# Optimization experiments

Measured on AMD Instinct MI355X. Metric: run time of the kernel, lower is better.

The kernel has to match this reference:

```python
import jax, jax.numpy as jnp
import numpy as np

TEMP = 0.7
B, V, C, H, W = 4, 2, 128, 32, 32  # V=2 views


def setup_inputs() -> dict:
    key = jax.random.key(0)
    k1, k2 = jax.random.split(key)
    feats = jax.random.normal(k1, (B, V, C, H, W), dtype=jnp.float32)
    # 'cos_dst' in the original implies L2-normalized embeddings along C
    feats = feats / jnp.linalg.norm(feats, axis=2, keepdims=True)
    labels = jax.random.randint(k2, (B, V, H, W), 0, 4, dtype=jnp.int32)
    return {"features": feats, "labels": labels}


def reference(features, labels):
    # split views on dim=1 and concat on batch (as in torch forward)
    f = jnp.concatenate([features[:, 0], features[:, 1]], axis=0)  # [2B, C, H, W]
    lab = jnp.concatenate([labels[:, 0], labels[:, 1]], axis=0)     # [2B, H, W]
    c = f.shape[1]
    # flatten pixels in (b, i, j) order -> [N, C]
    F_ = jnp.transpose(f, (0, 2, 3, 1)).reshape(-1, c)
    L_ = lab.reshape(-1)                                            # [N]
    # pairwise similarities: the triple loop's per-anchor 1x1 conv, batched
    S = jnp.einsum('nc,mc->nm', F_, F_) / TEMP                      # [N, N]
    diag = jnp.diagonal(S)                                          # self-contrast per anchor
    same = (L_[None, :] == L_[:, None]).astype(S.dtype)             # positives mask (incl. self)
    num = jnp.sum(same * S, axis=1) - diag
    den = jnp.sum(jnp.exp(S), axis=1) - jnp.exp(diag)
    cnt = jnp.sum(same, axis=1) - 1.0                               # mask.sum() - 1
    valid = (L_ != 0)                                               # x_label == 1 (label 0) skipped
    cnt_safe = jnp.where(valid, cnt, 1.0)
    loss_a = jnp.where(valid, jnp.log(den) - num / cnt_safe, 0.0)
    n_valid = jnp.sum(valid.astype(S.dtype))
    return jnp.where(n_valid > 0, jnp.sum(loss_a) / jnp.maximum(n_valid, 1.0), 0.0)
```

## Files before the change

kernel.cpp:

```cpp
#include <hip/hip_runtime.h>

#define TEMP 0.7f
#define LOG2E 1.4426950408889634f
#define LN2 0.6931471805599453f
#define NPIX 8192
#define CDIM 128
#define FSCALE 1.4356161f
#define EXPDIAG 4.1727352f

typedef __bf16 v8bf __attribute__((ext_vector_type(8)));
typedef float f32x4 __attribute__((ext_vector_type(4)));

#define OFF_ROWSUM 0
#define OFF_G      8192
#define OFF_COUNTS 8704
#define OFF_ACC    8708
#define OFF_ZERON  8712
#define OFF_SWF    8960

__global__ __launch_bounds__(256) void k0_zero(float* __restrict__ w) {
    const int i = blockIdx.x * 256 + threadIdx.x;
    if (i < OFF_ZERON) w[i] = 0.0f;
}

__global__ __launch_bounds__(256) void k1_build(
    const float* __restrict__ feats, const int* __restrict__ labels,
    v8bf* __restrict__ swf, float* __restrict__ G, int* __restrict__ counts)
{
    __shared__ float lds[128][65];
    __shared__ int lab_l[64];
    __shared__ float cs[2][4][128];

    const int t = threadIdx.x;
    const int lane = t & 63, cg = t >> 6;
    const int bp = blockIdx.x >> 4;
    const int pc = blockIdx.x & 15;
    const int b = bp & 3, v = bp >> 2;
    const int bv = b * 2 + v;
    const int p0 = pc * 64;
    const int nbase = bp * 1024 + p0;

    const float* src = feats + (size_t)bv * CDIM * 1024 + p0;
#pragma unroll
    for (int i = 0; i < 32; i++) {
        const int c = cg * 32 + i;
        lds[c][lane] = src[c * 1024 + lane];
    }
    if (t < 64) {
        const int lab = labels[bv * 1024 + p0 + t];
        lab_l[t] = lab;
#pragma unroll
        for (int k = 0; k < 4; k++) {
            unsigned long long m = __ballot(lab == k);
            if (t == 0) atomicAdd(&counts[k], (int)__popcll(m));
        }
    }
    __syncthreads();

    {
        const int cw = t & 127, h = t >> 7;
        float s0 = 0.f, s1 = 0.f, s2 = 0.f, s3 = 0.f;
#pragma unroll
        for (int i = 0; i < 32; i++) {
            const int nl = h * 32 + i;
            const int lab = lab_l[nl];
            const float f = lds[cw][nl];
            s0 += (lab == 0) ? f : 0.f;
            s1 += (lab == 1) ? f : 0.f;
            s2 += (lab == 2) ? f : 0.f;
            s3 += (lab == 3) ? f : 0.f;
        }
        cs[h][0][cw] = s0; cs[h][1][cw] = s1;
        cs[h][2][cw] = s2; cs[h][3][cw] = s3;
    }
    __syncthreads();
    if (t < 128) {
#pragma unroll
        for (int k = 0; k < 4; k++)
            atomicAdd(&G[k * CDIM + t], cs[0][k][t] + cs[1][k][t]);
    }

    #pragma unroll
    for (int i = 0; i < 4; i++) {
        const int slot = i * 256 + t;
        const int f = slot >> 6, l = slot & 63;
        const int ctl = f >> 2, kk = f & 3;
        const int q = l >> 4, r = l & 15;
        const int nl = ctl * 16 + r;
        const int c0 = kk * 32 + q * 8;
        v8bf val;
#pragma unroll
        for (int j = 0; j < 8; j++) val[j] = (__bf16)(lds[c0 + j][nl] * FSCALE);
        const int ctg = (nbase >> 4) + ctl;
        swf[(ctg * 4 + kk) * 64 + l] = val;
    }
}

__global__ __launch_bounds__(256, 4) void k3_gemm_expsum(
    const v8bf* __restrict__ swf, float* __restrict__ rowsum)
{
    const int lane = threadIdx.x & 63;
    const int wave = threadIdx.x >> 6;
    const int rowblk = blockIdx.x & 31;
    const int colchunk = blockIdx.x >> 5;
    const int rowbase = rowblk * 256 + wave * 64;
    const int rt0 = rowbase >> 4;

    v8bf a[4][4];
#pragma unroll
    for (int tt = 0; tt < 4; tt++)
#pragma unroll
        for (int kk = 0; kk < 4; kk++)
            a[tt][kk] = swf[((rt0 + tt) * 4 + kk) * 64 + lane];

    float rs[4][4];
#pragma unroll
    for (int tt = 0; tt < 4; tt++)
#pragma unroll
        for (int r = 0; r < 4; r++) rs[tt][r] = 0.f;

    const int ct0 = colchunk * 16;
    for (int ct = ct0; ct < ct0 + 16; ++ct) {
        const v8bf b0 = swf[(ct * 4 + 0) * 64 + lane];
        const v8bf b1 = swf[(ct * 4 + 1) * 64 + lane];
        const v8bf b2 = swf[(ct * 4 + 2) * 64 + lane];
        const v8bf b3 = swf[(ct * 4 + 3) * 64 + lane];
#pragma unroll
        for (int tt = 0; tt < 4; tt++) {
            f32x4 acc = {0.f, 0.f, 0.f, 0.f};
            acc = __builtin_amdgcn_mfma_f32_16x16x32_bf16(a[tt][0], b0, acc, 0, 0, 0);
            acc = __builtin_amdgcn_mfma_f32_16x16x32_bf16(a[tt][1], b1, acc, 0, 0, 0);
            acc = __builtin_amdgcn_mfma_f32_16x16x32_bf16(a[tt][2], b2, acc, 0, 0, 0);
            acc = __builtin_amdgcn_mfma_f32_16x16x32_bf16(a[tt][3], b3, acc, 0, 0, 0);
#pragma unroll
            for (int r = 0; r < 4; r++)
                rs[tt][r] += __builtin_amdgcn_exp2f(acc[r]);
        }
    }

#pragma unroll
    for (int m = 1; m < 16; m <<= 1)
#pragma unroll
        for (int tt = 0; tt < 4; tt++)
#pragma unroll
            for (int r = 0; r < 4; r++)
                rs[tt][r] += __shfl_xor(rs[tt][r], m, 64);

    if ((lane & 15) == 0) {
        const int g = lane >> 4;
#pragma unroll
        for (int tt = 0; tt < 4; tt++)
#pragma unroll
            for (int r = 0; r < 4; r++)
                atomicAdd(&rowsum[rowbase + tt * 16 + g * 4 + r], rs[tt][r]);
    }
}

__global__ __launch_bounds__(256) void k4_loss(
    const float* __restrict__ feats, const int* __restrict__ labels,
    const float* __restrict__ G, const int* __restrict__ counts,
    const float* __restrict__ rowsum, float* __restrict__ acc)
{
    __shared__ float pd[4][64];
    const int t = threadIdx.x, lane = t & 63, w = t >> 6;
    const int n0 = blockIdx.x * 64;
    const int bp = n0 >> 10, p0 = n0 & 1023;
    const int bv = ((bp & 3) << 1) + (bp >> 2);
    const int p = p0 + lane;
    const int lab = labels[(bv << 10) + p];

    const float* src = feats + (((size_t)bv * CDIM + w * 32) << 10) + p;
    const float* g0p = G + w * 32;
    float dot = 0.f;
#pragma unroll 8
    for (int c = 0; c < 32; ++c) {
        const float f = src[(size_t)c << 10];
        const float g0 = g0p[c], g1 = g0p[CDIM + c];
        const float g2 = g0p[2 * CDIM + c], g3 = g0p[3 * CDIM + c];
        const float g = (lab == 1) ? g1 : (lab == 2) ? g2 : (lab == 3) ? g3 : g0;
        dot += f * g;
    }
    pd[w][lane] = dot;
    __syncthreads();
    if (w == 0) {
        const float d = pd[0][lane] + pd[1][lane] + pd[2][lane] + pd[3][lane];
        float loss = 0.f;
        if (lab != 0) {
            const float num = (d - 1.0f) * (1.0f / TEMP);
            const float den = rowsum[n0 + lane] - EXPDIAG;
            const float cnt = (float)(counts[lab] - 1);
            loss = __builtin_amdgcn_logf(den) * LN2 - num / cnt;
        }
#pragma unroll
        for (int m = 1; m < 64; m <<= 1) loss += __shfl_xor(loss, m, 64);
        if (lane == 0) atomicAdd(acc, loss);
    }
}

__global__ void k5_final(const float* __restrict__ acc,
                         const int* __restrict__ counts,
                         float* __restrict__ out)
{
    const int nv = NPIX - counts[0];
    out[0] = (nv > 0) ? acc[0] / (float)nv : 0.0f;
}

extern "C" void kernel_launch(void* const* d_in, const int* in_sizes, int n_in,
                              void* d_out, int out_size, void* d_ws, size_t ws_size,
                              hipStream_t stream) {
    const float* feats = (const float*)d_in[0];
    const int* labels = (const int*)d_in[1];
    float* out = (float*)d_out;
    float* W = (float*)d_ws;

    float* rowsum = W + OFF_ROWSUM;
    float* G      = W + OFF_G;
    int*   counts = (int*)(W + OFF_COUNTS);
    float* acc    = W + OFF_ACC;
    v8bf*  swf    = (v8bf*)(W + OFF_SWF);

    k0_zero<<<(OFF_ZERON + 255) / 256, 256, 0, stream>>>(W);
    k1_build<<<128, 256, 0, stream>>>(feats, labels, swf, G, counts);
    k3_gemm_expsum<<<32 * 32, 256, 0, stream>>>(swf, rowsum);
    k4_loss<<<128, 256, 0, stream>>>(feats, labels, G, counts, rowsum, acc);
    k5_final<<<1, 1, 0, stream>>>(acc, counts, out);
}
```

Baseline: 47.27 us.

## Exploit Gram symmetry in exp-sum GEMM and fuse final reduction into loss kernel

The similarity-exp GEMM now covers only the upper-triangular 256x256 block pairs (528 blocks instead of 1024). Each off-diagonal block adds its exp values to both row sums and column sums via per-column shuffles and atomics, roughly halving the MFMA and exp2 work. In exchange it adds many more atomic adds and a serial loop to decode the block index. The build kernel is split into 256 blocks of 32 pixels for more parallelism. The final scalar kernel is folded into the loss kernel using a last-block-done counter, which removes one launch.

```diff
diff --git a/kernel.cpp b/kernel.cpp
--- a/kernel.cpp
+++ b/kernel.cpp
@@ -15,6 +15,7 @@
 #define OFF_G      8192
 #define OFF_COUNTS 8704
 #define OFF_ACC    8708
+#define OFF_DONE   8709
 #define OFF_ZERON  8712
 #define OFF_SWF    8960
 
@@ -27,26 +28,26 @@
     const float* __restrict__ feats, const int* __restrict__ labels,
     v8bf* __restrict__ swf, float* __restrict__ G, int* __restrict__ counts)
 {
-    __shared__ float lds[128][65];
-    __shared__ int lab_l[64];
+    __shared__ float lds[128][33];
+    __shared__ int lab_l[32];
     __shared__ float cs[2][4][128];
 
     const int t = threadIdx.x;
-    const int lane = t & 63, cg = t >> 6;
-    const int bp = blockIdx.x >> 4;
-    const int pc = blockIdx.x & 15;
+    const int bp = blockIdx.x >> 5;
+    const int pc = blockIdx.x & 31;
     const int b = bp & 3, v = bp >> 2;
     const int bv = b * 2 + v;
-    const int p0 = pc * 64;
+    const int p0 = pc * 32;
     const int nbase = bp * 1024 + p0;
 
     const float* src = feats + (size_t)bv * CDIM * 1024 + p0;
-#pragma unroll
-    for (int i = 0; i < 32; i++) {
-        const int c = cg * 32 + i;
-        lds[c][lane] = src[c * 1024 + lane];
-    }
-    if (t < 64) {
+    const int px = t & 31, c8 = t >> 5;
+#pragma unroll
+    for (int i = 0; i < 16; i++) {
+        const int c = i * 8 + c8;
+        lds[c][px] = src[c * 1024 + px];
+    }
+    if (t < 32) {
         const int lab = labels[bv * 1024 + p0 + t];
         lab_l[t] = lab;
 #pragma unroll
@@ -61,8 +62,8 @@
         const int cw = t & 127, h = t >> 7;
         float s0 = 0.f, s1 = 0.f, s2 = 0.f, s3 = 0.f;
 #pragma unroll
-        for (int i = 0; i < 32; i++) {
-            const int nl = h * 32 + i;
+        for (int i = 0; i < 16; i++) {
+            const int nl = h * 16 + i;
             const int lab = lab_l[nl];
             const float f = lds[cw][nl];
             s0 += (lab == 0) ? f : 0.f;
@@ -80,9 +81,9 @@
             atomicAdd(&G[k * CDIM + t], cs[0][k][t] + cs[1][k][t]);
     }
 
-    #pragma unroll
-    for (int i = 0; i < 4; i++) {
-        const int slot = i * 256 + t;
+#pragma unroll
+    for (int i2 = 0; i2 < 2; i2++) {
+        const int slot = i2 * 256 + t;
         const int f = slot >> 6, l = slot & 63;
         const int ctl = f >> 2, kk = f & 3;
         const int q = l >> 4, r = l & 15;
@@ -96,15 +97,19 @@
     }
 }
 
-__global__ __launch_bounds__(256, 4) void k3_gemm_expsum(
+__global__ __launch_bounds__(256, 2) void k3_gemm_expsum(
     const v8bf* __restrict__ swf, float* __restrict__ rowsum)
 {
     const int lane = threadIdx.x & 63;
     const int wave = threadIdx.x >> 6;
-    const int rowblk = blockIdx.x & 31;
-    const int colchunk = blockIdx.x >> 5;
-    const int rowbase = rowblk * 256 + wave * 64;
+    int rem = blockIdx.x, bi = 0;
+    while (rem >= 32 - bi) { rem -= 32 - bi; bi++; }
+    const int bj = bi + rem;
+    const bool offdiag = (bj != bi);
+    const int rowbase = bi * 256 + wave * 64;
+    const int colbase = bj * 256;
     const int rt0 = rowbase >> 4;
+    const int ct0 = colbase >> 4;
 
     v8bf a[4][4];
 #pragma unroll
@@ -119,12 +124,14 @@
 #pragma unroll
         for (int r = 0; r < 4; r++) rs[tt][r] = 0.f;
 
-    const int ct0 = colchunk * 16;
-    for (int ct = ct0; ct < ct0 + 16; ++ct) {
+#pragma unroll
+    for (int cl = 0; cl < 16; ++cl) {
+        const int ct = ct0 + cl;
         const v8bf b0 = swf[(ct * 4 + 0) * 64 + lane];
         const v8bf b1 = swf[(ct * 4 + 1) * 64 + lane];
         const v8bf b2 = swf[(ct * 4 + 2) * 64 + lane];
         const v8bf b3 = swf[(ct * 4 + 3) * 64 + lane];
+        float ccv = 0.f;
 #pragma unroll
         for (int tt = 0; tt < 4; tt++) {
             f32x4 acc = {0.f, 0.f, 0.f, 0.f};
@@ -133,8 +140,17 @@
             acc = __builtin_amdgcn_mfma_f32_16x16x32_bf16(a[tt][2], b2, acc, 0, 0, 0);
             acc = __builtin_amdgcn_mfma_f32_16x16x32_bf16(a[tt][3], b3, acc, 0, 0, 0);
 #pragma unroll
-            for (int r = 0; r < 4; r++)
-                rs[tt][r] += __builtin_amdgcn_exp2f(acc[r]);
+            for (int r = 0; r < 4; r++) {
+                const float e = __builtin_amdgcn_exp2f(acc[r]);
+                rs[tt][r] += e;
+                ccv += e;
+            }
+        }
+        if (offdiag) {
+            ccv += __shfl_xor(ccv, 16, 64);
+            ccv += __shfl_xor(ccv, 32, 64);
+            if (lane < 16)
+                atomicAdd(&rowsum[colbase + cl * 16 + lane], ccv);
         }
     }
 
@@ -159,7 +175,8 @@
 __global__ __launch_bounds__(256) void k4_loss(
     const float* __restrict__ feats, const int* __restrict__ labels,
     const float* __restrict__ G, const int* __restrict__ counts,
-    const float* __restrict__ rowsum, float* __restrict__ acc)
+    const float* __restrict__ rowsum, float* __restrict__ acc,
+    int* __restrict__ done, float* __restrict__ out)
 {
     __shared__ float pd[4][64];
     const int t = threadIdx.x, lane = t & 63, w = t >> 6;
@@ -193,16 +210,17 @@
         }
 #pragma unroll
         for (int m = 1; m < 64; m <<= 1) loss += __shfl_xor(loss, m, 64);
-        if (lane == 0) atomicAdd(acc, loss);
-    }
-}
-
-__global__ void k5_final(const float* __restrict__ acc,
-                         const int* __restrict__ counts,
-                         float* __restrict__ out)
-{
-    const int nv = NPIX - counts[0];
-    out[0] = (nv > 0) ? acc[0] / (float)nv : 0.0f;
+        if (lane == 0) {
+            atomicAdd(acc, loss);
+            __threadfence();
+            const int old = atomicAdd(done, 1);
+            if (old == 127) {
+                const float tot = atomicAdd(acc, 0.0f);
+                const int nv = NPIX - counts[0];
+                out[0] = (nv > 0) ? tot / (float)nv : 0.0f;
+            }
+        }
+    }
 }
 
 extern "C" void kernel_launch(void* const* d_in, const int* in_sizes, int n_in,
@@ -217,11 +235,11 @@
     float* G      = W + OFF_G;
     int*   counts = (int*)(W + OFF_COUNTS);
     float* acc    = W + OFF_ACC;
+    int*   done   = (int*)(W + OFF_DONE);
     v8bf*  swf    = (v8bf*)(W + OFF_SWF);
 
     k0_zero<<<(OFF_ZERON + 255) / 256, 256, 0, stream>>>(W);
-    k1_build<<<128, 256, 0, stream>>>(feats, labels, swf, G, counts);
-    k3_gemm_expsum<<<32 * 32, 256, 0, stream>>>(swf, rowsum);
-    k4_loss<<<128, 256, 0, stream>>>(feats, labels, G, counts, rowsum, acc);
-    k5_final<<<1, 1, 0, stream>>>(acc, counts, out);
-}
+    k1_build<<<256, 256, 0, stream>>>(feats, labels, swf, G, counts);
+    k3_gemm_expsum<<<528, 256, 0, stream>>>(swf, rowsum);
+    k4_loss<<<128, 256, 0, stream>>>(feats, labels, G, counts, rowsum, acc, done, out);
+}
```

Measured after the change: 91.59 us. 93.7% more time.

## Stage GEMM column tiles through LDS with double buffering; replace rowsum atomics with partials

Applied to the files above, without the earlier changes.

The exp-sum GEMM kernel now stages each column tile into a double-buffered LDS area using direct global-to-LDS loads, prefetching the next tile while the current one is used. Before, every wave loaded the same B tile from global memory separately. Per-row atomic adds into the row sums are replaced by plain stores into a per-column-chunk partial buffer, and the loss kernel reduces the 32 partials itself. This adds two barriers per iteration and a larger workspace, and the k0 zeroing no longer covers the partials, which is fine because they are fully overwritten.

```diff
diff --git a/kernel.cpp b/kernel.cpp
--- a/kernel.cpp
+++ b/kernel.cpp
@@ -11,12 +11,12 @@
 typedef __bf16 v8bf __attribute__((ext_vector_type(8)));
 typedef float f32x4 __attribute__((ext_vector_type(4)));
 
-#define OFF_ROWSUM 0
-#define OFF_G      8192
-#define OFF_COUNTS 8704
-#define OFF_ACC    8708
-#define OFF_ZERON  8712
-#define OFF_SWF    8960
+#define OFF_G      0
+#define OFF_COUNTS 512
+#define OFF_ACC    516
+#define OFF_ZERON  520
+#define OFF_PART   1024
+#define OFF_SWF    (1024 + 32 * NPIX)
 
 __global__ __launch_bounds__(256) void k0_zero(float* __restrict__ w) {
     const int i = blockIdx.x * 256 + threadIdx.x;
@@ -96,15 +96,28 @@
     }
 }
 
+__device__ __forceinline__ void stage_tile(const v8bf* swf, __bf16* ldsbase,
+                                           int ct, int wave, int lane)
+{
+    const char* g = (const char*)swf + ((size_t)ct << 12) + (wave << 10) + (lane << 4);
+    char* l = (char*)ldsbase + (wave << 10);
+    __builtin_amdgcn_global_load_lds(
+        (__attribute__((address_space(1))) void*)(char*)g,
+        (__attribute__((address_space(3))) void*)l, 16, 0, 0);
+}
+
 __global__ __launch_bounds__(256, 4) void k3_gemm_expsum(
-    const v8bf* __restrict__ swf, float* __restrict__ rowsum)
-{
-    const int lane = threadIdx.x & 63;
-    const int wave = threadIdx.x >> 6;
+    const v8bf* __restrict__ swf, float* __restrict__ part)
+{
+    __shared__ __align__(16) __bf16 bbuf[2][2048];
+    const int t = threadIdx.x;
+    const int lane = t & 63;
+    const int wave = t >> 6;
     const int rowblk = blockIdx.x & 31;
     const int colchunk = blockIdx.x >> 5;
     const int rowbase = rowblk * 256 + wave * 64;
     const int rt0 = rowbase >> 4;
+    const int ct0 = colchunk * 16;
 
     v8bf a[4][4];
 #pragma unroll
@@ -113,18 +126,29 @@
         for (int kk = 0; kk < 4; kk++)
             a[tt][kk] = swf[((rt0 + tt) * 4 + kk) * 64 + lane];
 
+    stage_tile(swf, &bbuf[0][0], ct0, wave, lane);
+
     float rs[4][4];
 #pragma unroll
     for (int tt = 0; tt < 4; tt++)
 #pragma unroll
         for (int r = 0; r < 4; r++) rs[tt][r] = 0.f;
 
-    const int ct0 = colchunk * 16;
-    for (int ct = ct0; ct < ct0 + 16; ++ct) {
-        const v8bf b0 = swf[(ct * 4 + 0) * 64 + lane];
-        const v8bf b1 = swf[(ct * 4 + 1) * 64 + lane];
-        const v8bf b2 = swf[(ct * 4 + 2) * 64 + lane];
-        const v8bf b3 = swf[(ct * 4 + 3) * 64 + lane];
+    for (int cl = 0; cl < 16; ++cl) {
+        if (cl < 15) {
+            stage_tile(swf, &bbuf[(cl + 1) & 1][0], ct0 + cl + 1, wave, lane);
+            asm volatile("s_waitcnt vmcnt(1)" ::: "memory");
+        } else {
+            asm volatile("s_waitcnt vmcnt(0)" ::: "memory");
+        }
+        __builtin_amdgcn_s_barrier();
+        asm volatile("" ::: "memory");
+
+        const v8bf* bb = (const v8bf*)&bbuf[cl & 1][0];
+        const v8bf b0 = bb[lane];
+        const v8bf b1 = bb[64 + lane];
+        const v8bf b2 = bb[128 + lane];
+        const v8bf b3 = bb[192 + lane];
 #pragma unroll
         for (int tt = 0; tt < 4; tt++) {
             f32x4 acc = {0.f, 0.f, 0.f, 0.f};
@@ -136,6 +160,8 @@
             for (int r = 0; r < 4; r++)
                 rs[tt][r] += __builtin_amdgcn_exp2f(acc[r]);
         }
+        asm volatile("s_waitcnt lgkmcnt(0)" ::: "memory");
+        __builtin_amdgcn_s_barrier();
     }
 
 #pragma unroll
@@ -148,18 +174,19 @@
 
     if ((lane & 15) == 0) {
         const int g = lane >> 4;
+        float* dst = part + (size_t)colchunk * NPIX + rowbase;
 #pragma unroll
         for (int tt = 0; tt < 4; tt++)
 #pragma unroll
             for (int r = 0; r < 4; r++)
-                atomicAdd(&rowsum[rowbase + tt * 16 + g * 4 + r], rs[tt][r]);
+                dst[tt * 16 + g * 4 + r] = rs[tt][r];
     }
 }
 
 __global__ __launch_bounds__(256) void k4_loss(
     const float* __restrict__ feats, const int* __restrict__ labels,
     const float* __restrict__ G, const int* __restrict__ counts,
-    const float* __restrict__ rowsum, float* __restrict__ acc)
+    const float* __restrict__ part, float* __restrict__ acc)
 {
     __shared__ float pd[4][64];
     const int t = threadIdx.x, lane = t & 63, w = t >> 6;
@@ -183,11 +210,14 @@
     pd[w][lane] = dot;
     __syncthreads();
     if (w == 0) {
+        float den = -EXPDIAG;
+#pragma unroll 8
+        for (int cc = 0; cc < 32; ++cc)
+            den += part[(size_t)cc * NPIX + n0 + lane];
         const float d = pd[0][lane] + pd[1][lane] + pd[2][lane] + pd[3][lane];
         float loss = 0.f;
         if (lab != 0) {
             const float num = (d - 1.0f) * (1.0f / TEMP);
-            const float den = rowsum[n0 + lane] - EXPDIAG;
             const float cnt = (float)(counts[lab] - 1);
             loss = __builtin_amdgcn_logf(den) * LN2 - num / cnt;
         }
@@ -213,15 +243,15 @@
     float* out = (float*)d_out;
     float* W = (float*)d_ws;
 
-    float* rowsum = W + OFF_ROWSUM;
     float* G      = W + OFF_G;
     int*   counts = (int*)(W + OFF_COUNTS);
     float* acc    = W + OFF_ACC;
+    float* part   = W + OFF_PART;
     v8bf*  swf    = (v8bf*)(W + OFF_SWF);
 
     k0_zero<<<(OFF_ZERON + 255) / 256, 256, 0, stream>>>(W);
     k1_build<<<128, 256, 0, stream>>>(feats, labels, swf, G, counts);
-    k3_gemm_expsum<<<32 * 32, 256, 0, stream>>>(swf, rowsum);
-    k4_loss<<<128, 256, 0, stream>>>(feats, labels, G, counts, rowsum, acc);
+    k3_gemm_expsum<<<32 * 32, 256, 0, stream>>>(swf, part);
+    k4_loss<<<128, 256, 0, stream>>>(feats, labels, G, counts, part, acc);
     k5_final<<<1, 1, 0, stream>>>(acc, counts, out);
 }
```

Result: slower. 107.7 us (+127.8%).

## Replace rowsum atomics with per-chunk partials, widen GEMM column chunks, split build finer

Applied to the files above, without the earlier changes.

The GEMM/exp-sum kernel now covers 32 column tiles per block in two interleaved MFMA chains, with a fully unrolled loop, half as many blocks and lower occupancy bounds. Instead of atomically adding row sums, each block writes plain stores into a per-column-chunk partial buffer, and the loss kernel sums the 16 partials per row. The build kernel is split into 256 blocks of 32 pixels for more parallelism. This removes float atomic contention and gives the scheduler independent MFMA chains, at the cost of extra partial-buffer traffic and higher register pressure.

```diff
diff --git a/kernel.cpp b/kernel.cpp
--- a/kernel.cpp
+++ b/kernel.cpp
@@ -11,12 +11,12 @@
 typedef __bf16 v8bf __attribute__((ext_vector_type(8)));
 typedef float f32x4 __attribute__((ext_vector_type(4)));
 
-#define OFF_ROWSUM 0
-#define OFF_G      8192
-#define OFF_COUNTS 8704
-#define OFF_ACC    8708
-#define OFF_ZERON  8712
-#define OFF_SWF    8960
+#define OFF_G      0
+#define OFF_COUNTS 512
+#define OFF_ACC    516
+#define OFF_ZERON  520
+#define OFF_PART   1024
+#define OFF_SWF    (1024 + 16 * NPIX)
 
 __global__ __launch_bounds__(256) void k0_zero(float* __restrict__ w) {
     const int i = blockIdx.x * 256 + threadIdx.x;
@@ -27,26 +27,26 @@
     const float* __restrict__ feats, const int* __restrict__ labels,
     v8bf* __restrict__ swf, float* __restrict__ G, int* __restrict__ counts)
 {
-    __shared__ float lds[128][65];
-    __shared__ int lab_l[64];
+    __shared__ float lds[128][33];
+    __shared__ int lab_l[32];
     __shared__ float cs[2][4][128];
 
     const int t = threadIdx.x;
-    const int lane = t & 63, cg = t >> 6;
-    const int bp = blockIdx.x >> 4;
-    const int pc = blockIdx.x & 15;
+    const int bp = blockIdx.x >> 5;
+    const int pc = blockIdx.x & 31;
     const int b = bp & 3, v = bp >> 2;
     const int bv = b * 2 + v;
-    const int p0 = pc * 64;
+    const int p0 = pc * 32;
     const int nbase = bp * 1024 + p0;
 
     const float* src = feats + (size_t)bv * CDIM * 1024 + p0;
-#pragma unroll
-    for (int i = 0; i < 32; i++) {
-        const int c = cg * 32 + i;
-        lds[c][lane] = src[c * 1024 + lane];
-    }
-    if (t < 64) {
+    const int px = t & 31, c8 = t >> 5;
+#pragma unroll
+    for (int i = 0; i < 16; i++) {
+        const int c = i * 8 + c8;
+        lds[c][px] = src[c * 1024 + px];
+    }
+    if (t < 32) {
         const int lab = labels[bv * 1024 + p0 + t];
         lab_l[t] = lab;
 #pragma unroll
@@ -61,8 +61,8 @@
         const int cw = t & 127, h = t >> 7;
         float s0 = 0.f, s1 = 0.f, s2 = 0.f, s3 = 0.f;
 #pragma unroll
-        for (int i = 0; i < 32; i++) {
-            const int nl = h * 32 + i;
+        for (int i = 0; i < 16; i++) {
+            const int nl = h * 16 + i;
             const int lab = lab_l[nl];
             const float f = lds[cw][nl];
             s0 += (lab == 0) ? f : 0.f;
@@ -80,9 +80,9 @@
             atomicAdd(&G[k * CDIM + t], cs[0][k][t] + cs[1][k][t]);
     }
 
-    #pragma unroll
-    for (int i = 0; i < 4; i++) {
-        const int slot = i * 256 + t;
+#pragma unroll
+    for (int i2 = 0; i2 < 2; i2++) {
+        const int slot = i2 * 256 + t;
         const int f = slot >> 6, l = slot & 63;
         const int ctl = f >> 2, kk = f & 3;
         const int q = l >> 4, r = l & 15;
@@ -96,8 +96,8 @@
     }
 }
 
-__global__ __launch_bounds__(256, 4) void k3_gemm_expsum(
-    const v8bf* __restrict__ swf, float* __restrict__ rowsum)
+__global__ __launch_bounds__(256, 2) void k3_gemm_expsum(
+    const v8bf* __restrict__ swf, float* __restrict__ part)
 {
     const int lane = threadIdx.x & 63;
     const int wave = threadIdx.x >> 6;
@@ -105,6 +105,7 @@
     const int colchunk = blockIdx.x >> 5;
     const int rowbase = rowblk * 256 + wave * 64;
     const int rt0 = rowbase >> 4;
+    const int ct0 = colchunk * 32;
 
     v8bf a[4][4];
 #pragma unroll
@@ -119,22 +120,28 @@
 #pragma unroll
         for (int r = 0; r < 4; r++) rs[tt][r] = 0.f;
 
-    const int ct0 = colchunk * 16;
-    for (int ct = ct0; ct < ct0 + 16; ++ct) {
-        const v8bf b0 = swf[(ct * 4 + 0) * 64 + lane];
-        const v8bf b1 = swf[(ct * 4 + 1) * 64 + lane];
-        const v8bf b2 = swf[(ct * 4 + 2) * 64 + lane];
-        const v8bf b3 = swf[(ct * 4 + 3) * 64 + lane];
+#pragma unroll
+    for (int it = 0; it < 16; ++it) {
+        const v8bf* pA = swf + (size_t)(ct0 + it) * 256 + lane;
+        const v8bf* pB = swf + (size_t)(ct0 + 16 + it) * 256 + lane;
+        const v8bf bA0 = pA[0], bA1 = pA[64], bA2 = pA[128], bA3 = pA[192];
+        const v8bf bB0 = pB[0], bB1 = pB[64], bB2 = pB[128], bB3 = pB[192];
 #pragma unroll
         for (int tt = 0; tt < 4; tt++) {
-            f32x4 acc = {0.f, 0.f, 0.f, 0.f};
-            acc = __builtin_amdgcn_mfma_f32_16x16x32_bf16(a[tt][0], b0, acc, 0, 0, 0);
-            acc = __builtin_amdgcn_mfma_f32_16x16x32_bf16(a[tt][1], b1, acc, 0, 0, 0);
-            acc = __builtin_amdgcn_mfma_f32_16x16x32_bf16(a[tt][2], b2, acc, 0, 0, 0);
-            acc = __builtin_amdgcn_mfma_f32_16x16x32_bf16(a[tt][3], b3, acc, 0, 0, 0);
+            f32x4 accA = {0.f, 0.f, 0.f, 0.f};
+            f32x4 accB = {0.f, 0.f, 0.f, 0.f};
+            accA = __builtin_amdgcn_mfma_f32_16x16x32_bf16(a[tt][0], bA0, accA, 0, 0, 0);
+            accA = __builtin_amdgcn_mfma_f32_16x16x32_bf16(a[tt][1], bA1, accA, 0, 0, 0);
+            accA = __builtin_amdgcn_mfma_f32_16x16x32_bf16(a[tt][2], bA2, accA, 0, 0, 0);
+            accA = __builtin_amdgcn_mfma_f32_16x16x32_bf16(a[tt][3], bA3, accA, 0, 0, 0);
+            accB = __builtin_amdgcn_mfma_f32_16x16x32_bf16(a[tt][0], bB0, accB, 0, 0, 0);
+            accB = __builtin_amdgcn_mfma_f32_16x16x32_bf16(a[tt][1], bB1, accB, 0, 0, 0);
+            accB = __builtin_amdgcn_mfma_f32_16x16x32_bf16(a[tt][2], bB2, accB, 0, 0, 0);
+            accB = __builtin_amdgcn_mfma_f32_16x16x32_bf16(a[tt][3], bB3, accB, 0, 0, 0);
 #pragma unroll
             for (int r = 0; r < 4; r++)
-                rs[tt][r] += __builtin_amdgcn_exp2f(acc[r]);
+                rs[tt][r] += __builtin_amdgcn_exp2f(accA[r])
+                           + __builtin_amdgcn_exp2f(accB[r]);
         }
     }
 
@@ -148,18 +155,19 @@
 
     if ((lane & 15) == 0) {
         const int g = lane >> 4;
+        float* dst = part + (size_t)colchunk * NPIX + rowbase;
 #pragma unroll
         for (int tt = 0; tt < 4; tt++)
 #pragma unroll
             for (int r = 0; r < 4; r++)
-                atomicAdd(&rowsum[rowbase + tt * 16 + g * 4 + r], rs[tt][r]);
+                dst[tt * 16 + g * 4 + r] = rs[tt][r];
     }
 }
 
 __global__ __launch_bounds__(256) void k4_loss(
     const float* __restrict__ feats, const int* __restrict__ labels,
     const float* __restrict__ G, const int* __restrict__ counts,
-    const float* __restrict__ rowsum, float* __restrict__ acc)
+    const float* __restrict__ part, float* __restrict__ acc)
 {
     __shared__ float pd[4][64];
     const int t = threadIdx.x, lane = t & 63, w = t >> 6;
@@ -183,11 +191,14 @@
     pd[w][lane] = dot;
     __syncthreads();
     if (w == 0) {
+        float den = -EXPDIAG;
+#pragma unroll
+        for (int cc = 0; cc < 16; ++cc)
+            den += part[(size_t)cc * NPIX + n0 + lane];
         const float d = pd[0][lane] + pd[1][lane] + pd[2][lane] + pd[3][lane];
         float loss = 0.f;
         if (lab != 0) {
             const float num = (d - 1.0f) * (1.0f / TEMP);
-            const float den = rowsum[n0 + lane] - EXPDIAG;
             const float cnt = (float)(counts[lab] - 1);
             loss = __builtin_amdgcn_logf(den) * LN2 - num / cnt;
         }
@@ -213,15 +224,15 @@
     float* out = (float*)d_out;
     float* W = (float*)d_ws;
 
-    float* rowsum = W + OFF_ROWSUM;
     float* G      = W + OFF_G;
     int*   counts = (int*)(W + OFF_COUNTS);
     float* acc    = W + OFF_ACC;
+    float* part   = W + OFF_PART;
     v8bf*  swf    = (v8bf*)(W + OFF_SWF);
 
     k0_zero<<<(OFF_ZERON + 255) / 256, 256, 0, stream>>>(W);
-    k1_build<<<128, 256, 0, stream>>>(feats, labels, swf, G, counts);
-    k3_gemm_expsum<<<32 * 32, 256, 0, stream>>>(swf, rowsum);
-    k4_loss<<<128, 256, 0, stream>>>(feats, labels, G, counts, rowsum, acc);
+    k1_build<<<256, 256, 0, stream>>>(feats, labels, swf, G, counts);
+    k3_gemm_expsum<<<32 * 16, 256, 0, stream>>>(swf, part);
+    k4_loss<<<128, 256, 0, stream>>>(feats, labels, G, counts, part, acc);
     k5_final<<<1, 1, 0, stream>>>(acc, counts, out);
 }
```

After: 79.95 us. +69.1%, slower.
